# Kernel tuning notes

Measured on AMD Instinct MI355X. Metric: run time of the kernel, lower is better.

## Reference

```python
import jax, jax.numpy as jnp
import numpy as np

MAX_BOXES_PER_IMAGE = 200
NMS_IOU_THRESHOLD = 0.45
CONFIDENCE_THRESHOLD = 0.01
NEG = jnp.float32(-1e9)

B, N, C = 32, 24564, 81  # batch, anchors, classes (incl background)


def setup_inputs() -> dict:
    key = jax.random.key(0)
    k1, k2, k3 = jax.random.split(key, 3)
    logits = jax.random.normal(k1, (B, N, 4 + C), dtype=jnp.float32)
    # anchors in corner format [x0, y0, x1, y1], valid boxes in [0,1]
    centers = jax.random.uniform(k2, (N, 2), dtype=jnp.float32)
    sizes = jax.random.uniform(k3, (N, 2), dtype=jnp.float32) * 0.3 + 0.02
    anchors = jnp.clip(jnp.concatenate([centers - sizes / 2, centers + sizes / 2], axis=-1), 0.0, 1.0)
    return {"logits": logits, "anchors": anchors}


def decode_boxes(loc, anchors):
    # anchors [N,4] corners -> center/size; loc [B,N,4] offsets (no variance scaling, per source)
    cxcy = (anchors[:, 2:4] + anchors[:, 0:2]) / 2  # [N,2]
    wh = anchors[:, 2:4] - anchors[:, 0:2]          # [N,2]
    ctr = loc[..., 0:2] * wh + cxcy                 # [B,N,2]
    sz = jnp.exp(loc[..., 2:4]) * wh                # [B,N,2]
    boxes = jnp.concatenate([ctr - sz / 2, ctr + sz / 2], axis=-1)
    return jnp.clip(boxes, 0.0, 1.0)


def nms_single(boxes, scores):
    # boxes [N,4] corners, scores [N] (already -inf for background / below-threshold)
    area = (boxes[:, 2] - boxes[:, 0]) * (boxes[:, 3] - boxes[:, 1])

    def step(s, _):
        i = jnp.argmax(s)
        keep = s[i] > NEG / 2
        b = boxes[i]
        lt = jnp.maximum(b[:2], boxes[:, :2])
        rb = jnp.minimum(b[2:], boxes[:, 2:])
        whi = jnp.clip(rb - lt, 0.0)
        inter = whi[:, 0] * whi[:, 1]
        iou = inter / (area[i] + area - inter + 1e-9)
        s = jnp.where(iou > NMS_IOU_THRESHOLD, NEG, s).at[i].set(NEG)
        return s, (i, keep)

    _, (idx, keep) = jax.lax.scan(step, scores, None, length=MAX_BOXES_PER_IMAGE)
    return idx, keep  # [M], [M]


def reference(logits, anchors):
    loc = logits[..., :4]
    cls = jax.nn.softmax(logits[..., 4:], axis=-1)          # [B,N,C]
    scores = jnp.max(cls, axis=-1)                           # [B,N]
    classes = jnp.argmax(cls, axis=-1)                       # [B,N]
    boxes = decode_boxes(loc, anchors)                       # [B,N,4]
    # emulate boolean_mask(classes != 0) + score_threshold by masking scores
    valid = (classes != 0) & (scores >= CONFIDENCE_THRESHOLD)
    masked = jnp.where(valid, scores, NEG)
    idx, keep = jax.vmap(nms_single)(boxes, masked)          # [B,M]
    det_boxes = jax.vmap(lambda b, i: b[i])(boxes, idx) * keep[..., None].astype(boxes.dtype)
    det_scores = jax.vmap(lambda s, i: s[i])(scores, idx) * keep.astype(scores.dtype)
    det_classes = jax.vmap(lambda c, i: c[i])(classes, idx) * keep.astype(classes.dtype)
    det_num = jnp.sum(keep, axis=-1).astype(jnp.int32)
    return det_boxes, det_classes, det_scores, det_num
```

## Files before the change

kernel.cpp:

```cpp
#include <hip/hip_runtime.h>

#define Bn 32
#define Nn 24564
#define MAXB 200
#define NBIN 2048
#define CH 2048
#define NCHK 4
#define CHK_PRE 3
#define CHTOT (NCHK * CH)
#define CHPRE (CHK_PRE * CH)
#define INVK 0xFFFFFFFFu
#define NITER 24

typedef unsigned long long u64;
typedef unsigned int u32;

__device__ inline double fast_exp_d(double x) {
  const double LOG2E = 1.4426950408889634074;
  const double LN2   = 0.69314718055994530942;
  double t = x * LOG2E;
  double fi = floor(t + 0.5);
  double f = (t - fi) * LN2;
  double p = 2.505210838544172e-8;
  p = p * f + 2.755731922398589e-7;
  p = p * f + 2.7557319223985893e-6;
  p = p * f + 2.48015873015873e-5;
  p = p * f + 1.984126984126984e-4;
  p = p * f + 1.3888888888888889e-3;
  p = p * f + 8.333333333333333e-3;
  p = p * f + 4.1666666666666664e-2;
  p = p * f + 1.6666666666666666e-1;
  p = p * f + 0.5;
  p = p * f + 1.0;
  p = p * f + 1.0;
  long long e = (long long)fi;
  return p * __longlong_as_double((e + 1023LL) << 52);
}

__device__ inline double clip01(double v) {
  return v < 0.0 ? 0.0 : (v > 1.0 ? 1.0 : v);
}

__global__ __launch_bounds__(256) void z1_score(const float* __restrict__ logits,
                                                u32* __restrict__ keyA) {
  const int tid = threadIdx.x;
  const int bx = blockIdx.x;
  const int b = bx / 384;
  const int n0 = (bx % 384) << 6;
  const int g = tid >> 2, s = tid & 3;
  const int n = n0 + g;
  if (n >= Nn) return;
  const float* row = logits + ((size_t)b * Nn + n) * 85;

  float rv[21];
  float mx = -1e30f; int ai = 1000;
  #pragma unroll
  for (int q = 0; q < 21; ++q) {
    int c = s + 4 * q;
    float v = (c < 81) ? row[4 + c] : -1e30f;
    rv[q] = v;
    if (c < 81 && v > mx) { mx = v; ai = c; }
  }
  #pragma unroll
  for (int d = 1; d <= 2; d <<= 1) {
    float om = __shfl_xor(mx, d);
    int oi = __shfl_xor(ai, d);
    if (om > mx || (om == mx && oi < ai)) { mx = om; ai = oi; }
  }
  float sum = 0.f;
  #pragma unroll
  for (int q = 0; q < 21; ++q) {
    if (s + 4 * q < 81) sum += __expf(rv[q] - mx);
  }
  sum += __shfl_xor(sum, 1);
  sum += __shfl_xor(sum, 2);
  if (s == 0) {
    float sc = 1.0f / sum;
    u32 kv = INVK;
    if (ai != 0 && sc >= 0.00985f) kv = ~__float_as_uint(sc);
    keyA[(size_t)b * Nn + n] = kv;
  }
}

__global__ __launch_bounds__(1024) void z3_cutcompact(const u32* __restrict__ keyA,
                                                      int* __restrict__ chunkCntG,
                                                      int* __restrict__ clist) {
  __shared__ int hist[NBIN];
  __shared__ int chunkIdL[NBIN];
  __shared__ int wsum[16];
  __shared__ int sBinHi;
  __shared__ int sCnt[NCHK];
  const int b = blockIdx.x;
  const int tid = threadIdx.x;
  const int lane = tid & 63, wid = tid >> 6;
  const u32* kb = keyA + (size_t)b * Nn;

  u32 kvreg[NITER];
  #pragma unroll
  for (int it = 0; it < NITER; ++it) {
    int i = it * 1024 + tid;
    kvreg[it] = (i < Nn) ? kb[i] : INVK;
  }

  for (int i = tid; i < NBIN; i += 1024) hist[i] = 0;
  chunkIdL[2 * tid] = 255;
  chunkIdL[2 * tid + 1] = 255;
  if (tid < NCHK) sCnt[tid] = 0;
  __syncthreads();

  #pragma unroll
  for (int it = 0; it < NITER; ++it) {
    u32 bin = (kvreg[it] - 0xC0000000u) >> 15;
    if (bin < NBIN) atomicAdd(&hist[bin], 1);
  }
  __syncthreads();

  int h0 = hist[2 * tid], h1 = hist[2 * tid + 1];
  int v = h0 + h1;
  int iv = v;
  #pragma unroll
  for (int d = 1; d < 64; d <<= 1) {
    int t = __shfl_up(iv, d);
    if (lane >= d) iv += t;
  }
  if (lane == 63) wsum[wid] = iv;
  __syncthreads();
  if (tid < 16) {
    int w = wsum[tid];
    #pragma unroll
    for (int d = 1; d < 16; d <<= 1) {
      int t = __shfl_up(w, d);
      if ((int)tid >= d) w += t;
    }
    wsum[tid] = w;
  }
  __syncthreads();
  int excl = iv - v + (wid > 0 ? wsum[wid - 1] : 0);
  hist[2 * tid] = excl + h0;
  hist[2 * tid + 1] = excl + h0 + h1;
  __syncthreads();

  int binLo = -1, cumBase = 0;
  for (int c = 0; c < NCHK; ++c) {
    if (tid == 0) sBinHi = binLo;
    __syncthreads();
    const int limit = cumBase + CH;
    int loc = -1;
    if (hist[2 * tid] <= limit) loc = 2 * tid;
    if (hist[2 * tid + 1] <= limit) loc = 2 * tid + 1;
    if (loc > binLo) atomicMax(&sBinHi, loc);
    __syncthreads();
    int binHi = sBinHi;
    if (binHi == binLo) binHi = binLo + 1;
    if (2 * tid > binLo && 2 * tid <= binHi) chunkIdL[2 * tid] = c;
    if (2 * tid + 1 > binLo && 2 * tid + 1 <= binHi) chunkIdL[2 * tid + 1] = c;
    cumBase = hist[(binHi < NBIN ? binHi : NBIN - 1)];
    binLo = binHi;
    __syncthreads();
  }

  #pragma unroll 1
  for (int it = 0; it < NITER; ++it) {
    int i = it * 1024 + tid;
    int c = 255;
    u32 bin = (kvreg[it] - 0xC0000000u) >> 15;
    if (i < Nn && bin < NBIN) c = chunkIdL[bin];
    #pragma unroll
    for (int cc = 0; cc < NCHK; ++cc) {
      bool pred = (c == cc);
      u64 m = __ballot(pred);
      if (m) {
        int base = 0;
        if (lane == 0) base = atomicAdd(&sCnt[cc], (int)__popcll(m));
        base = __shfl(base, 0);
        if (pred) {
          int off = (int)__popcll(m & ((1ULL << lane) - 1ULL));
          int p = base + off;
          if (p < CH) clist[b * CHTOT + cc * CH + p] = i;
        }
      }
    }
  }
  __syncthreads();
  if (tid < NCHK) chunkCntG[b * NCHK + tid] = sCnt[tid];
}

__global__ __launch_bounds__(256) void z4_rescore(const float* __restrict__ logits,
                                                  const float* __restrict__ anchors,
                                                  const int* __restrict__ clist,
                                                  const int* __restrict__ chunkCntG,
                                                  double* __restrict__ boxesd,
                                                  int* __restrict__ clsd,
                                                  u64* __restrict__ ekeysG) {
  __shared__ u64 ekseg[256];
  const int tid = threadIdx.x;
  const int bx = blockIdx.x;
  const int b = bx / (CHK_PRE * 8);
  const int blk = bx % (CHK_PRE * 8);
  const int c = blk >> 3;
  const int seg = blk & 7;
  int cnt = chunkCntG[b * NCHK + c];
  cnt = cnt > CH ? CH : cnt;
  const int g = tid >> 2, s = tid & 3;

  #pragma unroll 1
  for (int pass = 0; pass < 4; ++pass) {
    const int slot = seg * 256 + pass * 64 + g;
    u64 K = ~0ULL;
    if (slot < cnt) {
      const int n = clist[b * CHTOT + c * CH + slot];
      const float* row = logits + ((size_t)b * Nn + n) * 85;
      float rv[21];
      float mx = -1e30f; int ai = 1000;
      #pragma unroll
      for (int q = 0; q < 21; ++q) {
        int cc = s + 4 * q;
        float vv = (cc < 81) ? row[4 + cc] : -1e30f;
        rv[q] = vv;
        if (cc < 81 && vv > mx) { mx = vv; ai = cc; }
      }
      #pragma unroll
      for (int d = 1; d <= 2; d <<= 1) {
        float om = __shfl_xor(mx, d);
        int oi = __shfl_xor(ai, d);
        if (om > mx || (om == mx && oi < ai)) { mx = om; ai = oi; }
      }
      double sum = 0.0;
      #pragma unroll
      for (int q = 0; q < 21; ++q) {
        if (s + 4 * q < 81) sum += fast_exp_d((double)rv[q] - (double)mx);
      }
      sum += __shfl_xor(sum, 1);
      sum += __shfl_xor(sum, 2);
      if (s == 0) {
        double score = 1.0 / sum;
        if (ai != 0 && score >= 0.01) {
          float4 a4 = reinterpret_cast<const float4*>(anchors)[n];
          double ax1 = a4.x, ay1 = a4.y, ax2 = a4.z, ay2 = a4.w;
          double cx = (ax2 + ax1) * 0.5, cy = (ay2 + ay1) * 0.5;
          double ww = ax2 - ax1, hh = ay2 - ay1;
          double ctrx = (double)row[0] * ww + cx;
          double ctry = (double)row[1] * hh + cy;
          double szx = fast_exp_d((double)row[2]) * ww;
          double szy = fast_exp_d((double)row[3]) * hh;
          double* bp = boxesd + (size_t)(b * Nn + n) * 4;
          bp[0] = clip01(ctrx - szx * 0.5);
          bp[1] = clip01(ctry - szy * 0.5);
          bp[2] = clip01(ctrx + szx * 0.5);
          bp[3] = clip01(ctry + szy * 0.5);
          clsd[b * Nn + n] = ai;
          u64 sb2 = (u64)__double_as_longlong(score);
          u64 e4 = (sb2 >> 52) - 1015ULL;
          u64 mant45 = (sb2 & ((1ULL << 52) - 1)) >> 7;
          u64 flip = (~((e4 << 45) | mant45)) & ((1ULL << 49) - 1);
          K = (flip << 15) | (u64)n;
        }
      }
    }
    if (s == 0) ekseg[pass * 64 + g] = K;
  }
  __syncthreads();

  for (int k = 2; k <= 256; k <<= 1) {
    for (int j = k >> 1; j >= 1; j >>= 1) {
      if (tid < 128) {
        int l = ((tid & ~(j - 1)) << 1) | (tid & (j - 1));
        int r = l | j;
        bool up = ((l & k) == 0);
        u64 a = ekseg[l], bv = ekseg[r];
        if ((a > bv) == up) { ekseg[l] = bv; ekseg[r] = a; }
      }
      __syncthreads();
    }
  }
  u64* dstp = ekeysG + (size_t)b * CHPRE + c * CH + seg * 256;
  for (int i = tid; i < 256; i += 256) dstp[i] = ekseg[i];
}

__global__ __launch_bounds__(1024) void z5_sortnms(const float* __restrict__ logits,
                                                   const float* __restrict__ anchors,
                                                   const u64* __restrict__ ekeysG,
                                                   const int* __restrict__ chunkCntG,
                                                   const int* __restrict__ clist,
                                                   double* __restrict__ boxesd,
                                                   int* __restrict__ clsd,
                                                   float* __restrict__ out) {
  __shared__ u64 ek[CH];
  __shared__ double bbuf[2][64][4];
  __shared__ u64 awv[16];
  __shared__ u64 killm[64];
  __shared__ double selBox[MAXB][4];
  __shared__ double selArea[MAXB];
  __shared__ float selScore[MAXB];
  __shared__ int selIdx[MAXB];
  __shared__ int sS;
  const int b = blockIdx.x;
  const int tid = threadIdx.x;
  const int lane = tid & 63, wid = tid >> 6;
  const double THR = 0.45;
  if (tid == 0) sS = 0;
  __syncthreads();

  for (int c = 0; c < NCHK; ++c) {
    if (sS >= MAXB) break;
    int cnt = chunkCntG[b * NCHK + c];
    cnt = cnt > CH ? CH : cnt;
    if (cnt == 0) break;

    if (c < CHK_PRE) {
      for (int i = tid; i < CH; i += 1024) ek[i] = ekeysG[(size_t)b * CHPRE + c * CH + i];
      __syncthreads();
      for (int L = 256; L <= 1024; L <<= 1) {
        int pair = tid / L, i = tid % L;
        int base = pair * 2 * L;
        int l = base + i, r = base + 2 * L - 1 - i;
        u64 a = ek[l], bv = ek[r];
        if (a > bv) { ek[l] = bv; ek[r] = a; }
        __syncthreads();
        for (int j = L >> 1; j >= 1; j >>= 1) {
          int ll = ((tid & ~(j - 1)) << 1) | (tid & (j - 1));
          int rr = ll | j;
          u64 x = ek[ll], y = ek[rr];
          if (x > y) { ek[ll] = y; ek[rr] = x; }
          __syncthreads();
        }
      }
    } else {
      for (int i = tid; i < CH; i += 1024) ek[i] = ~0ULL;
      __syncthreads();
      const int g = tid >> 2, s4 = tid & 3;
      #pragma unroll 1
      for (int pass = 0; pass < CH / 256; ++pass) {
        int slot = pass * 256 + g;
        if (slot < cnt) {
          const int n = clist[b * CHTOT + c * CH + slot];
          const float* row = logits + ((size_t)b * Nn + n) * 85;
          float rv[21];
          float mx = -1e30f; int ai = 1000;
          #pragma unroll
          for (int q = 0; q < 21; ++q) {
            int cc = s4 + 4 * q;
            float vv = (cc < 81) ? row[4 + cc] : -1e30f;
            rv[q] = vv;
            if (cc < 81 && vv > mx) { mx = vv; ai = cc; }
          }
          #pragma unroll
          for (int d = 1; d <= 2; d <<= 1) {
            float om = __shfl_xor(mx, d);
            int oi = __shfl_xor(ai, d);
            if (om > mx || (om == mx && oi < ai)) { mx = om; ai = oi; }
          }
          double sum = 0.0;
          #pragma unroll
          for (int q = 0; q < 21; ++q) {
            if (s4 + 4 * q < 81) sum += fast_exp_d((double)rv[q] - (double)mx);
          }
          sum += __shfl_xor(sum, 1);
          sum += __shfl_xor(sum, 2);
          if (s4 == 0) {
            u64 K = ~0ULL;
            double score = 1.0 / sum;
            if (ai != 0 && score >= 0.01) {
              float4 a4 = reinterpret_cast<const float4*>(anchors)[n];
              double ax1 = a4.x, ay1 = a4.y, ax2 = a4.z, ay2 = a4.w;
              double cx = (ax2 + ax1) * 0.5, cy = (ay2 + ay1) * 0.5;
              double ww = ax2 - ax1, hh = ay2 - ay1;
              double ctrx = (double)row[0] * ww + cx;
              double ctry = (double)row[1] * hh + cy;
              double szx = fast_exp_d((double)row[2]) * ww;
              double szy = fast_exp_d((double)row[3]) * hh;
              double* bp = boxesd + (size_t)(b * Nn + n) * 4;
              bp[0] = clip01(ctrx - szx * 0.5);
              bp[1] = clip01(ctry - szy * 0.5);
              bp[2] = clip01(ctrx + szx * 0.5);
              bp[3] = clip01(ctry + szy * 0.5);
              clsd[b * Nn + n] = ai;
              u64 sb2 = (u64)__double_as_longlong(score);
              u64 e4 = (sb2 >> 52) - 1015ULL;
              u64 mant45 = (sb2 & ((1ULL << 52) - 1)) >> 7;
              u64 flip = (~((e4 << 45) | mant45)) & ((1ULL << 49) - 1);
              K = (flip << 15) | (u64)n;
            }
            ek[slot] = K;
          }
        }
      }
      __syncthreads();
      int P2 = 64;
      while (P2 < cnt) P2 <<= 1;
      for (int k = 2; k <= P2; k <<= 1) {
        for (int j = k >> 1; j >= 1; j >>= 1) {
          if (tid < (P2 >> 1)) {
            int l = ((tid & ~(j - 1)) << 1) | (tid & (j - 1));
            int r = l | j;
            bool up = ((l & k) == 0);
            u64 a = ek[l], bbv = ek[r];
            if ((a > bbv) == up) { ek[l] = bbv; ek[r] = a; }
          }
          __syncthreads();
        }
      }
    }

    int pos = 0, bf = 0;
    if (tid < 256) {
      int ci = tid >> 2, comp = tid & 3;
      u64 Kc = ek[ci];
      double vv = 0.0;
      if (Kc != ~0ULL) vv = boxesd[(size_t)(b * Nn + (int)(Kc & 0x7FFF)) * 4 + comp];
      bbuf[0][ci][comp] = vv;
    }
    __syncthreads();
    for (;;) {
      int S = sS;
      if (S >= MAXB || pos >= CH) break;
      u64 K = ek[pos + lane];
      bool valid = (K != ~0ULL);
      if (!__any(valid)) break;

      if (tid < 256 && pos + 64 < CH) {
        int ci = tid >> 2, comp = tid & 3;
        u64 Kc = ek[pos + 64 + ci];
        double vv = 0.0;
        if (Kc != ~0ULL) vv = boxesd[(size_t)(b * Nn + (int)(Kc & 0x7FFF)) * 4 + comp];
        bbuf[bf ^ 1][ci][comp] = vv;
      }

      double cx1 = bbuf[bf][lane][0], cy1 = bbuf[bf][lane][1];
      double cx2 = bbuf[bf][lane][2], cy2 = bbuf[bf][lane][3];
      double carea = (cx2 - cx1) * (cy2 - cy1);

      bool aliveL = true;
      for (int k = wid; k < S; k += 16) {
        double ltx = fmax(selBox[k][0], cx1), lty = fmax(selBox[k][1], cy1);
        double rbx = fmin(selBox[k][2], cx2), rby = fmin(selBox[k][3], cy2);
        double w = rbx - ltx; w = w < 0 ? 0 : w;
        double h = rby - lty; h = h < 0 ? 0 : h;
        double inter = w * h;
        double denom = selArea[k] + carea - inter + 1e-9;
        if (inter > THR * denom) aliveL = false;
      }
      u64 aw = __ballot(aliveL);
      if (lane == 0) awv[wid] = aw;

      #pragma unroll
      for (int q = 0; q < 4; ++q) {
        int j = (wid << 2) | q;
        double jx1 = bbuf[bf][j][0], jy1 = bbuf[bf][j][1];
        double jx2 = bbuf[bf][j][2], jy2 = bbuf[bf][j][3];
        double jar = (jx2 - jx1) * (jy2 - jy1);
        double ltx = fmax(jx1, cx1), lty = fmax(jy1, cy1);
        double rbx = fmin(jx2, cx2), rby = fmin(jy2, cy2);
        double w = rbx - ltx; w = w < 0 ? 0 : w;
        double h = rby - lty; h = h < 0 ? 0 : h;
        double inter = w * h;
        double denom = jar + carea - inter + 1e-9;
        u64 km = __ballot(inter > THR * denom);
        if (lane == 0) killm[j] = km;
      }
      __syncthreads();

      if (tid < 64) {
        u64 alive = __ballot(valid);
        #pragma unroll
        for (int w = 0; w < 16; ++w) alive &= awv[w];
        u64 m = alive;
        int Sl = S;
        while (m != 0 && Sl < MAXB) {
          int j = __ffsll((unsigned long long)m) - 1;
          if (lane == 0) {
            double jx1 = bbuf[bf][j][0], jy1 = bbuf[bf][j][1];
            double jx2 = bbuf[bf][j][2], jy2 = bbuf[bf][j][3];
            u64 Kj = ek[pos + j];
            u64 key49 = (~(Kj >> 15)) & ((1ULL << 49) - 1);
            u64 e = (key49 >> 45) + 1015ULL;
            u64 mant = (key49 & ((1ULL << 45) - 1)) << 7;
            selBox[Sl][0] = jx1; selBox[Sl][1] = jy1;
            selBox[Sl][2] = jx2; selBox[Sl][3] = jy2;
            selArea[Sl] = (jx2 - jx1) * (jy2 - jy1);
            selScore[Sl] = (float)__longlong_as_double((long long)((e << 52) | mant));
            selIdx[Sl] = (int)(Kj & 0x7FFF);
          }
          Sl++;
          m &= ~(1ULL << j);
          m &= ~killm[j];
        }
        if (lane == 0) sS = Sl;
      }
      __syncthreads();
      bf ^= 1;
      pos += 64;
    }
    __syncthreads();
  }

  const int S = sS;
  float* det_boxes = out;
  float* det_classes = out + Bn * MAXB * 4;
  float* det_scores = out + Bn * MAXB * 4 + Bn * MAXB;
  float* det_num = out + Bn * MAXB * 4 + 2 * Bn * MAXB;
  for (int k = tid; k < MAXB; k += 1024) {
    int o = b * MAXB + k;
    if (k < S) {
      det_boxes[o * 4 + 0] = (float)selBox[k][0];
      det_boxes[o * 4 + 1] = (float)selBox[k][1];
      det_boxes[o * 4 + 2] = (float)selBox[k][2];
      det_boxes[o * 4 + 3] = (float)selBox[k][3];
      det_classes[o] = (float)clsd[b * Nn + selIdx[k]];
      det_scores[o] = selScore[k];
    } else {
      det_boxes[o * 4 + 0] = 0.f; det_boxes[o * 4 + 1] = 0.f;
      det_boxes[o * 4 + 2] = 0.f; det_boxes[o * 4 + 3] = 0.f;
      det_classes[o] = 0.f;
      det_scores[o] = 0.f;
    }
  }
  if (tid == 0) det_num[b] = (float)S;
}

extern "C" void kernel_launch(void* const* d_in, const int* in_sizes, int n_in,
                              void* d_out, int out_size, void* d_ws, size_t ws_size,
                              hipStream_t stream) {
  const float* logits = (const float*)d_in[0];
  const float* anchors = (const float*)d_in[1];
  float* out = (float*)d_out;
  char* ws = (char*)d_ws;

  double* boxesd = (double*)ws;
  size_t off = (size_t)Bn * Nn * 4 * sizeof(double);
  int* clsd    = (int*)(ws + off);  off += (size_t)Bn * Nn * sizeof(int);
  u32* keyA    = (u32*)(ws + off);  off += (size_t)Bn * Nn * sizeof(u32);
  int* chunkCnt= (int*)(ws + off);  off += (size_t)Bn * NCHK * sizeof(int);
  int* clist   = (int*)(ws + off);  off += (size_t)Bn * CHTOT * sizeof(int);
  u64* ekeysG  = (u64*)(ws + off);

  z1_score     <<<dim3(Bn * 384),        dim3(256),  0, stream>>>(logits, keyA);
  z3_cutcompact<<<dim3(Bn),              dim3(1024), 0, stream>>>(keyA, chunkCnt, clist);
  z4_rescore   <<<dim3(Bn * CHK_PRE * 8),dim3(256),  0, stream>>>(logits, anchors, clist,
                                                                  chunkCnt, boxesd, clsd, ekeysG);
  z5_sortnms   <<<dim3(Bn),              dim3(1024), 0, stream>>>(logits, anchors, ekeysG,
                                                                  chunkCnt, clist, boxesd,
                                                                  clsd, out);
}
```

Measured before the change: 154.4 us.

## Process NMS candidates in 128-wide batches with whole-chunk SoA box staging

```diff
diff --git a/kernel.cpp b/kernel.cpp
--- a/kernel.cpp
+++ b/kernel.cpp
@@ -286,9 +286,9 @@
                                                    int* __restrict__ clsd,
                                                    float* __restrict__ out) {
   __shared__ u64 ek[CH];
-  __shared__ double bbuf[2][64][4];
+  __shared__ double cbX1[CH], cbY1[CH], cbX2[CH], cbY2[CH];
   __shared__ u64 awv[16];
-  __shared__ u64 killm[64];
+  __shared__ u64 killmLo[128], killmHi[128];
   __shared__ double selBox[MAXB][4];
   __shared__ double selArea[MAXB];
   __shared__ float selScore[MAXB];
@@ -402,36 +402,33 @@
       }
     }
 
-    int pos = 0, bf = 0;
-    if (tid < 256) {
-      int ci = tid >> 2, comp = tid & 3;
-      u64 Kc = ek[ci];
-      double vv = 0.0;
-      if (Kc != ~0ULL) vv = boxesd[(size_t)(b * Nn + (int)(Kc & 0x7FFF)) * 4 + comp];
-      bbuf[0][ci][comp] = vv;
+    for (int i = tid; i < CH; i += 1024) {
+      u64 Kc = ek[i];
+      double x1 = 0.0, y1 = 0.0, x2 = 0.0, y2 = 0.0;
+      if (Kc != ~0ULL) {
+        const double* bp = boxesd + (size_t)(b * Nn + (int)(Kc & 0x7FFF)) * 4;
+        x1 = bp[0]; y1 = bp[1]; x2 = bp[2]; y2 = bp[3];
+      }
+      cbX1[i] = x1; cbY1[i] = y1; cbX2[i] = x2; cbY2[i] = y2;
     }
     __syncthreads();
+
+    const int half = wid >> 3;
+    const int wsub = wid & 7;
+    int pos = 0;
     for (;;) {
       int S = sS;
       if (S >= MAXB || pos >= CH) break;
-      u64 K = ek[pos + lane];
-      bool valid = (K != ~0ULL);
-      if (!__any(valid)) break;
-
-      if (tid < 256 && pos + 64 < CH) {
-        int ci = tid >> 2, comp = tid & 3;
-        u64 Kc = ek[pos + 64 + ci];
-        double vv = 0.0;
-        if (Kc != ~0ULL) vv = boxesd[(size_t)(b * Nn + (int)(Kc & 0x7FFF)) * 4 + comp];
-        bbuf[bf ^ 1][ci][comp] = vv;
-      }
-
-      double cx1 = bbuf[bf][lane][0], cy1 = bbuf[bf][lane][1];
-      double cx2 = bbuf[bf][lane][2], cy2 = bbuf[bf][lane][3];
+      bool anyLo = __any(ek[pos + lane] != ~0ULL);
+      if (!anyLo) break;
+
+      const int cc = half * 64 + lane;
+      double cx1 = cbX1[pos + cc], cy1 = cbY1[pos + cc];
+      double cx2 = cbX2[pos + cc], cy2 = cbY2[pos + cc];
       double carea = (cx2 - cx1) * (cy2 - cy1);
 
       bool aliveL = true;
-      for (int k = wid; k < S; k += 16) {
+      for (int k = wsub; k < S; k += 8) {
         double ltx = fmax(selBox[k][0], cx1), lty = fmax(selBox[k][1], cy1);
         double rbx = fmin(selBox[k][2], cx2), rby = fmin(selBox[k][3], cy2);
         double w = rbx - ltx; w = w < 0 ? 0 : w;
@@ -443,34 +440,51 @@
       u64 aw = __ballot(aliveL);
       if (lane == 0) awv[wid] = aw;
 
+      double lx1 = cbX1[pos + lane], ly1 = cbY1[pos + lane];
+      double lx2 = cbX2[pos + lane], ly2 = cbY2[pos + lane];
+      double lar = (lx2 - lx1) * (ly2 - ly1);
+      double hx1 = cbX1[pos + 64 + lane], hy1 = cbY1[pos + 64 + lane];
+      double hx2 = cbX2[pos + 64 + lane], hy2 = cbY2[pos + 64 + lane];
+      double har = (hx2 - hx1) * (hy2 - hy1);
+
       #pragma unroll
-      for (int q = 0; q < 4; ++q) {
-        int j = (wid << 2) | q;
-        double jx1 = bbuf[bf][j][0], jy1 = bbuf[bf][j][1];
-        double jx2 = bbuf[bf][j][2], jy2 = bbuf[bf][j][3];
+      for (int q = 0; q < 8; ++q) {
+        int j = (wid << 3) | q;
+        double jx1 = cbX1[pos + j], jy1 = cbY1[pos + j];
+        double jx2 = cbX2[pos + j], jy2 = cbY2[pos + j];
         double jar = (jx2 - jx1) * (jy2 - jy1);
-        double ltx = fmax(jx1, cx1), lty = fmax(jy1, cy1);
-        double rbx = fmin(jx2, cx2), rby = fmin(jy2, cy2);
+        double ltx = fmax(jx1, lx1), lty = fmax(jy1, ly1);
+        double rbx = fmin(jx2, lx2), rby = fmin(jy2, ly2);
         double w = rbx - ltx; w = w < 0 ? 0 : w;
         double h = rby - lty; h = h < 0 ? 0 : h;
         double inter = w * h;
-        double denom = jar + carea - inter + 1e-9;
-        u64 km = __ballot(inter > THR * denom);
-        if (lane == 0) killm[j] = km;
+        double denom = jar + lar - inter + 1e-9;
+        u64 kmLo = __ballot(inter > THR * denom);
+        ltx = fmax(jx1, hx1); lty = fmax(jy1, hy1);
+        rbx = fmin(jx2, hx2); rby = fmin(jy2, hy2);
+        w = rbx - ltx; w = w < 0 ? 0 : w;
+        h = rby - lty; h = h < 0 ? 0 : h;
+        inter = w * h;
+        denom = jar + har - inter + 1e-9;
+        u64 kmHi = __ballot(inter > THR * denom);
+        if (lane == 0) { killmLo[j] = kmLo; killmHi[j] = kmHi; }
       }
       __syncthreads();
 
       if (tid < 64) {
-        u64 alive = __ballot(valid);
+        u64 m0 = __ballot(ek[pos + lane] != ~0ULL);
+        u64 m1 = __ballot(ek[pos + 64 + lane] != ~0ULL);
         #pragma unroll
-        for (int w = 0; w < 16; ++w) alive &= awv[w];
-        u64 m = alive;
+        for (int w = 0; w < 8; ++w)  m0 &= awv[w];
+        #pragma unroll
+        for (int w = 8; w < 16; ++w) m1 &= awv[w];
         int Sl = S;
-        while (m != 0 && Sl < MAXB) {
-          int j = __ffsll((unsigned long long)m) - 1;
+        while ((m0 | m1) != 0 && Sl < MAXB) {
+          int j = m0 ? (__ffsll((unsigned long long)m0) - 1)
+                     : (64 + __ffsll((unsigned long long)m1) - 1);
           if (lane == 0) {
-            double jx1 = bbuf[bf][j][0], jy1 = bbuf[bf][j][1];
-            double jx2 = bbuf[bf][j][2], jy2 = bbuf[bf][j][3];
+            double jx1 = cbX1[pos + j], jy1 = cbY1[pos + j];
+            double jx2 = cbX2[pos + j], jy2 = cbY2[pos + j];
             u64 Kj = ek[pos + j];
             u64 key49 = (~(Kj >> 15)) & ((1ULL << 49) - 1);
             u64 e = (key49 >> 45) + 1015ULL;
@@ -482,14 +496,14 @@
             selIdx[Sl] = (int)(Kj & 0x7FFF);
           }
           Sl++;
-          m &= ~(1ULL << j);
-          m &= ~killm[j];
+          if (j < 64) m0 &= ~(1ULL << j); else m1 &= ~(1ULL << (j - 64));
+          m0 &= ~killmLo[j];
+          m1 &= ~killmHi[j];
         }
         if (lane == 0) sS = Sl;
       }
       __syncthreads();
-      bf ^= 1;
-      pos += 64;
+      pos += 128;
     }
     __syncthreads();
   }
```

Measured after the change: 183.7 us. 19.0% more time.
